# Performance work log

Measured on AMD Instinct MI355X. Metric: run time of the kernel, lower is better.

Reference implementation:

```python
import jax, jax.numpy as jnp
import numpy as np

NA, NO = 3, 85  # anchors per level, nc+5
OUT = NA * NO   # 255


def _p(key, shape):
    return jax.random.normal(key, shape, dtype=jnp.float32) * 0.02


def setup_inputs() -> dict:
    key = jax.random.key(0)
    ks = jax.random.split(key, 12)
    return {
        'x0': jax.random.normal(ks[0], (8, 128, 160, 160), jnp.float32),
        'x1': jax.random.normal(ks[1], (8, 256, 80, 80), jnp.float32),
        'x2': jax.random.normal(ks[2], (8, 512, 40, 40), jnp.float32),
        'x3': jax.random.normal(ks[3], (8, 1024, 20, 20), jnp.float32),
        # CLLABlock 1x1 convs (weight stored as [out_ch, in_ch])
        'w_conv1': _p(ks[4], (128, 128)), 'b_conv1': jnp.zeros((128,), jnp.float32),
        'w_conv2': _p(ks[5], (128, 256)), 'b_conv2': jnp.zeros((128,), jnp.float32),
        # CLLA q/k/v Linear layers (torch Linear: [out_feat, in_feat])
        'wq': _p(ks[6], (128, 128)), 'bq': jnp.zeros((128,), jnp.float32),
        'wk': _p(ks[7], (128, 128)), 'bk': jnp.zeros((128,), jnp.float32),
        'wv': _p(ks[8], (128, 128)), 'bv': jnp.zeros((128,), jnp.float32),
        # det head conv and extra level convs m[0], m[1]
        'w_det': _p(ks[9], (OUT, 128)), 'b_det': jnp.zeros((OUT,), jnp.float32),
        'wm0': _p(ks[10], (OUT, 512)), 'bm0': jnp.zeros((OUT,), jnp.float32),
        'wm1': _p(ks[11], (OUT, 1024)), 'bm1': jnp.zeros((OUT,), jnp.float32),
    }


def _conv1x1(x, w, b):
    # x: [b,c,h,w], w: [o,c]
    return jnp.einsum('bchw,oc->bohw', x, w) + b[None, :, None, None]


def _clla(f1, f2, wq, bq, wk, bk, wv, bv):
    # f1: [b,c,2H,2W] (fine), f2: [b,c,H,W] (coarse); range=2 -> pad=0
    b, c, H, W = f2.shape
    # torch loop: local[n] = f1[..., i::2, j::2], n = i*2+j, stacked on a new axis,
    # then permute(0,3,4,2,1) -> [b,H,W,4,c]
    loc = f1.reshape(b, c, H, 2, W, 2).transpose(0, 2, 4, 3, 5, 1).reshape(b, H, W, 4, c)
    x2_ = f2.transpose(0, 2, 3, 1)              # [b,H,W,c]
    q = x2_ @ wq.T + bq                          # [b,H,W,c]
    k = loc @ wk.T + bk                          # [b,H,W,4,c]
    v = loc @ wv.T + bv                          # [b,H,W,4,c]
    dots = jnp.einsum('bhwc,bhwnc->bhwn', q, k) / 2.0  # /range
    irr = 2.0 * jnp.mean(dots, axis=-1, keepdims=True) - dots
    att = jax.nn.softmax(irr, axis=-1)           # [b,H,W,4]
    out = jnp.einsum('bhwn,bhwnc->bhwc', att, v).transpose(0, 3, 1, 2)  # [b,c,H,W]
    return (out + f2) / 2.0


def _reshape_head(p):
    bs, _, ny, nx = p.shape
    return p.reshape(bs, NA, NO, ny, nx).transpose(0, 1, 3, 4, 2)  # [bs,na,ny,nx,no]


def reference(x0, x1, x2, x3,
              w_conv1, b_conv1, w_conv2, b_conv2,
              wq, bq, wk, bk, wv, bv,
              w_det, b_det, wm0, bm0, wm1, bm1):
    # training-mode forward of CLLADetect: returns raw head outputs p
    f1 = _conv1x1(x0, w_conv1, b_conv1)
    f2 = _conv1x1(x1, w_conv2, b_conv2)
    f = _clla(f1, f2, wq, bq, wk, bk, wv, bv)
    p0 = _reshape_head(_conv1x1(f, w_det, b_det))   # [8,3,80,80,85]
    p1 = _reshape_head(_conv1x1(x2, wm0, bm0))      # [8,3,40,40,85]
    p2 = _reshape_head(_conv1x1(x3, wm1, bm1))      # [8,3,20,20,85]
    return (p0, p1, p2)
```

## Files before the change

kernel.cpp:

```cpp
#include <hip/hip_runtime.h>

typedef unsigned short u16;
typedef unsigned int   u32;
typedef __bf16 bf16x8 __attribute__((ext_vector_type(8)));
typedef float  f32x4  __attribute__((ext_vector_type(4)));

__device__ __forceinline__ u16 f2bf(float f){
  u32 u = __float_as_uint(f);
  return (u16)((u + 0x7FFFu + ((u >> 16) & 1u)) >> 16);
}
__device__ __forceinline__ float bf2f(u16 h){ return __uint_as_float(((u32)h) << 16); }

#define WS_A1    0u
#define WS_WM0   196608u
#define WS_WM1   458752u
#define WS_WDVC  983040u
#define WS_C1    1048576u
#define WS_BM0   1051136u
#define WS_BM1   1052160u
#define WS_T     1053184u
#define WS_U     1184256u
#define WS_P     1184768u
#define WS_W6    1316352u
#define WS_U6    1381888u
#define WS_R     1382400u

__device__ __forceinline__ size_t wimg_off(int n, int k, int BN, int nK){
  int nt = n / BN, r = n % BN, kt = k >> 6;
  int slot = (((k & 63) >> 3) ^ (r & 7));
  return (size_t)(nt * nK + kt) * (size_t)(BN * 128) + (size_t)r * 128 + (slot << 4) + (k & 7) * 2;
}

__global__ __launch_bounds__(256) void prepA_k(const float* __restrict__ wq, const float* __restrict__ bq,
                                               const float* __restrict__ wc2, const float* __restrict__ bc2,
                                               const float* __restrict__ wk,  const float* __restrict__ wv,
                                               const float* __restrict__ wc1, const float* __restrict__ bc1,
                                               const float* __restrict__ bv,  char* ws)
{
  const int blk = blockIdx.x, j = threadIdx.x;
  if (blk < 128){
    int a = blk;
    float s = 0.f;
    for (int c = 0; c < 128; c++) s += wq[a * 128 + c] * wc2[c * 256 + j];
    ((float*)(ws + WS_T))[a * 256 + j] = s;
    if (j == 0){
      float su = bq[a];
      for (int c = 0; c < 128; c++) su += wq[a * 128 + c] * bc2[c];
      ((float*)(ws + WS_U))[a] = su;
    }
  } else if (blk < 256){
    int n = blk - 128;
    if (j < 128){
      float s = 0.f;
      for (int c = 0; c < 128; c++) s += wk[n * 128 + c] * wc1[c * 128 + j];
      ((float*)(ws + WS_P))[n * 128 + j] = s;
    }
  } else {
    int n = blk - 256;
    if (j < 128){
      float s = 0.f;
      for (int c = 0; c < 128; c++) s += wv[n * 128 + c] * wc1[c * 128 + j];
      ((float*)(ws + WS_W6))[n * 128 + j] = s;
    }
    if (j == 0){
      float s = bv[n];
      for (int c = 0; c < 128; c++) s += wv[n * 128 + c] * bc1[c];
      ((float*)(ws + WS_U6))[n] = s;
    }
  }
}

__global__ __launch_bounds__(256) void prep2_k(
    const float* __restrict__ wc2,
    const float* __restrict__ wdet, const float* __restrict__ bdet,
    const float* __restrict__ wm0, const float* __restrict__ bm0,
    const float* __restrict__ wm1, const float* __restrict__ bm1,
    const float* __restrict__ bc2, char* ws)
{
  const float* T  = (const float*)(ws + WS_T);
  const float* u  = (const float*)(ws + WS_U);
  const float* P  = (const float*)(ws + WS_P);
  const float* W6 = (const float*)(ws + WS_W6);
  const float* U6 = (const float*)(ws + WS_U6);
  int idx = blockIdx.x * 256 + threadIdx.x;
  if (idx < 98304){
    int n = idx >> 8, k = idx & 255;
    float s = 0.f;
    if (n < 128){
      for (int i = 0; i < 128; i++) s += P[i * 128 + n] * T[i * 256 + k];
      s *= 0.5f;
    } else if (n < 383){
      int oc = n - 128;
      for (int c = 0; c < 128; c++) s += wdet[oc * 128 + c] * wc2[c * 256 + k];
      s *= 0.5f;
    }
    *(u16*)(ws + WS_A1 + wimg_off(n, k, 128, 4)) = f2bf(s);
  } else if (idx < 98688){
    int n = idx - 98304;
    float s = 0.f;
    if (n < 128){
      for (int i = 0; i < 128; i++) s += P[i * 128 + n] * u[i];
      s *= 0.5f;
    } else if (n < 383){
      int oc = n - 128;
      float ss = 0.f;
      for (int c = 0; c < 128; c++) ss += wdet[oc * 128 + c] * (bc2[c] + U6[c]);
      s = bdet[oc] + 0.5f * ss;
    }
    ((float*)(ws + WS_C1))[n] = s;
  } else if (idx < 131456){
    int id = idx - 98688; int n = id >> 7, k = id & 127;
    float s = 0.f;
    if (n < 255){
      for (int c = 0; c < 128; c++) s += wdet[n * 128 + c] * W6[c * 128 + k];
      s *= 0.5f;
    }
    ((u16*)(ws + WS_WDVC))[n * 128 + k] = f2bf(s);
  } else if (idx < 262528){
    int id = idx - 131456; int n = id >> 9, k = id & 511;
    float s = (n < 255) ? wm0[n * 512 + k] : 0.f;
    *(u16*)(ws + WS_WM0 + wimg_off(n, k, 256, 8)) = f2bf(s);
  } else if (idx < 524672){
    int id = idx - 262528; int n = id >> 10, k = id & 1023;
    float s = (n < 255) ? wm1[n * 1024 + k] : 0.f;
    *(u16*)(ws + WS_WM1 + wimg_off(n, k, 256, 16)) = f2bf(s);
  } else if (idx < 525184){
    int id = idx - 524672;
    if (id < 256) ((float*)(ws + WS_BM0))[id] = (id < 255) ? bm0[id] : 0.f;
    else { int n = id - 256; ((float*)(ws + WS_BM1))[n] = (n < 255) ? bm1[n] : 0.f; }
  }
}

template<int Kd, int BM, int BN, int WM, int WN, int PPB, int Cin, int EPI, int ROWB>
__device__ __forceinline__ void gemm_body(char* lds, int mt, int nt,
                                          const float* __restrict__ Ap, const char* __restrict__ wimg,
                                          const float* __restrict__ bias, void* __restrict__ outp, long out_off)
{
  constexpr int nK = Kd / 64;
  constexpr int NV = BM / 16;
  char* ldsA = lds;
  char* ldsW = lds + BM * 128;
  const int t = threadIdx.x;
  const int lane = t & 63;
  const int wid = t >> 6;
  const int wm = wid / WN, wn = wid % WN;
  const int m0 = mt * BM, n0 = nt * BN;
  const int lr = lane & 15, lg = lane >> 4;
  f32x4 acc[4][4] = {};

  const int q = t & 3, chl = t >> 2;
  const int chunkA = chl >> 3, elo = (chl & 7) * 2;

  for (int kt = 0; kt < nK; kt++){
    {
      const int c = kt * 64 + chl;
      float4 v4[NV];
      #pragma unroll
      for (int v = 0; v < NV; v++){
        int pg = m0 + v * 16 + q * 4;
        int bb = pg / PPB, pp = pg - bb * PPB;
        v4[v] = *(const float4*)(Ap + (size_t)bb * Cin * PPB + (size_t)c * PPB + pp);
      }
      #pragma unroll
      for (int v = 0; v < NV; v++){
        #pragma unroll
        for (int e = 0; e < 4; e++){
          int pi = v * 16 + q * 4 + e;
          float val = ((const float*)&v4[v])[e];
          *(u16*)(ldsA + pi * 128 + ((chunkA ^ (pi & 7)) << 4) + elo) = f2bf(val);
        }
      }
    }
    {
      const char* srct = wimg + (size_t)(nt * nK + kt) * (BN * 128);
      #pragma unroll
      for (int it = 0; it < BN / 32; it++){
        int off = t * 16 + it * 4096;
        *(uint4*)(ldsW + off) = *(const uint4*)(srct + off);
      }
    }
    __syncthreads();
    #pragma unroll
    for (int ks = 0; ks < 2; ks++){
      bf16x8 af[4], bfr[4];
      #pragma unroll
      for (int i = 0; i < 4; i++){
        int r = wm * 64 + i * 16 + lr;
        af[i] = *(const bf16x8*)(ldsA + r * 128 + ((((ks << 2) + lg) ^ (r & 7)) << 4));
      }
      #pragma unroll
      for (int j = 0; j < 4; j++){
        int r = wn * 64 + j * 16 + lr;
        bfr[j] = *(const bf16x8*)(ldsW + r * 128 + ((((ks << 2) + lg) ^ (r & 7)) << 4));
      }
      #pragma unroll
      for (int i = 0; i < 4; i++)
        #pragma unroll
        for (int j = 0; j < 4; j++)
          acc[i][j] = __builtin_amdgcn_mfma_f32_16x16x32_bf16(af[i], bfr[j], acc[i][j], 0, 0, 0);
    }
    __syncthreads();
  }

  if constexpr (EPI == 0){
    u16* lds2 = (u16*)lds;
    #pragma unroll
    for (int j = 0; j < 4; j++){
      int nl = wn * 64 + j * 16 + lr;
      float bs = bias[n0 + nl];
      #pragma unroll
      for (int i = 0; i < 4; i++){
        #pragma unroll
        for (int r = 0; r < 4; r++){
          int ml = wm * 64 + i * 16 + lg * 4 + r;
          lds2[ml * 136 + nl] = f2bf(acc[i][j][r] + bs);
        }
      }
    }
    __syncthreads();
    char* outb = (char*)outp;
    #pragma unroll
    for (int it = 0; it < BM / 16; it++){
      int idx = it * 256 + t;
      int row = idx >> 4, c16 = idx & 15;
      *(uint4*)(outb + (size_t)(m0 + row) * ROWB + n0 * 2 + c16 * 16) =
          *(const uint4*)((const char*)lds2 + row * 272 + c16 * 16);
    }
  } else {
    #pragma unroll
    for (int j = 0; j < 4; j++){
      int nn = n0 + wn * 64 + j * 16 + lr;
      float bs = bias[nn];
      #pragma unroll
      for (int i = 0; i < 4; i++){
        #pragma unroll
        for (int r = 0; r < 4; r++){
          int mm = m0 + wm * 64 + i * 16 + lg * 4 + r;
          float v = acc[i][j][r] + bs;
          if (nn < 255){
            int b = mm / PPB, p = mm - b * PPB;
            int a = nn / 85, o = nn - a * 85;
            ((float*)outp)[out_off + ((size_t)(b * 3 + a) * PPB + p) * 85 + o] = v;
          }
        }
      }
    }
  }
}

__global__ __launch_bounds__(256) void gemms_k(const float* __restrict__ x1,
                                               const float* __restrict__ x2,
                                               const float* __restrict__ x3,
                                               char* __restrict__ ws,
                                               float* __restrict__ out)
{
  __shared__ char lds[40960];
  const int bid = blockIdx.x;
  if (bid < 50){
    gemm_body<1024, 64, 256, 1, 4, 400, 1024, 2, 0>(lds, bid, 0,
        x3, ws + WS_WM1, (const float*)(ws + WS_BM1), out, 16320000L);
  } else if (bid < 250){
    gemm_body<512, 64, 256, 1, 4, 1600, 512, 2, 0>(lds, bid - 50, 0,
        x2, ws + WS_WM0, (const float*)(ws + WS_BM0), out, 13056000L);
  } else {
    int b2 = bid - 250;
    gemm_body<256, 128, 128, 2, 2, 6400, 256, 0, 768>(lds, b2 / 3, b2 % 3,
        x1, ws + WS_A1, (const float*)(ws + WS_C1), ws + WS_R, 0L);
  }
}

__global__ __launch_bounds__(256) void clla_k(const float* __restrict__ x0,
                                              const char* __restrict__ ws,
                                              float* __restrict__ out)
{
  __shared__ char smem[29184];
  char* x0s = smem;
  char* rs  = smem + 16384;
  char* h0s = smem + 20480;
  float* stg = (float*)smem;

  const char* Rb   = ws + WS_R;
  const char* wdvi = ws + WS_WDVC;

  const int t = threadIdx.x;
  const int lane = t & 63, wid = t >> 6;
  const int lr = lane & 15, lg = lane >> 4;
  const int blk = blockIdx.x;
  const int b = blk / 400, rem = blk % 400;
  const int h = rem / 5, w0 = (rem % 5) * 16;
  const int c0 = b * 6400 + h * 80 + w0;
  const int pr = h * 80 + w0;

  {
    const int ch = t >> 1, r = t & 1;
    const float* gp = x0 + ((size_t)b * 128 + ch) * 25600
                    + (size_t)(2 * h + r) * 160 + 2 * w0;
    float4 v4[8];
    #pragma unroll
    for (int i = 0; i < 8; i++) v4[i] = *(const float4*)(gp + i * 4);
    const int chunk = ch >> 3, elo = (ch & 7) * 2;
    #pragma unroll
    for (int i = 0; i < 8; i++){
      #pragma unroll
      for (int e = 0; e < 4; e++){
        int j = i * 4 + e;
        int fr = ((j >> 1) << 2) + r * 2 + (j & 1);
        float val = ((const float*)&v4[i])[e];
        *(u16*)(x0s + fr * 256 + (((chunk ^ ((fr & 7) << 1)) & 15) << 4) + elo) = f2bf(val);
      }
    }
    const int lc2 = t >> 4, c2 = t & 15;
    *(uint4*)(rs + lc2 * 256 + (((c2 ^ ((lc2 & 7) << 1)) & 15) << 4)) =
        *(const uint4*)(Rb + (size_t)(c0 + lc2) * 768 + c2 * 16);
    #pragma unroll
    for (int i = 0; i < 2; i++){
      int idx = i * 256 + t;
      int row = idx >> 5, c16 = idx & 31;
      *(uint4*)(h0s + row * 544 + c16 * 16) =
          *(const uint4*)(Rb + (size_t)(c0 + row) * 768 + 256 + c16 * 16);
    }
  }
  __syncthreads();

  float myatt;
  {
    const int px = t >> 4, n = (t >> 2) & 3, cq2 = t & 3;
    const int fr = px * 4 + n;
    float d = 0.f;
    #pragma unroll
    for (int g = 0; g < 4; g++){
      int c = cq2 * 4 + g;
      bf16x8 rv = *(const bf16x8*)(rs  + px * 256 + (((c ^ ((px & 7) << 1)) & 15) << 4));
      bf16x8 fv = *(const bf16x8*)(x0s + fr * 256 + (((c ^ ((fr & 7) << 1)) & 15) << 4));
      #pragma unroll
      for (int e = 0; e < 8; e++) d += (float)rv[e] * (float)fv[e];
    }
    d += __shfl_xor(d, 1); d += __shfl_xor(d, 2);
    float s4 = d + __shfl_xor(d, 4); s4 += __shfl_xor(s4, 8);
    float irr = 0.5f * s4 - d;
    float mx = fmaxf(irr, __shfl_xor(irr, 4)); mx = fmaxf(mx, __shfl_xor(mx, 8));
    float e1 = __expf(irr - mx);
    float den = e1 + __shfl_xor(e1, 4); den += __shfl_xor(den, 8);
    myatt = e1 / den;
  }

  {
    const int px = t >> 4, cp = t & 15;
    float o[8];
    #pragma unroll
    for (int e = 0; e < 8; e++) o[e] = 0.f;
    #pragma unroll
    for (int n = 0; n < 4; n++){
      float a = __shfl(myatt, (t & 48) | (n << 2));
      int fr = px * 4 + n;
      bf16x8 fv = *(const bf16x8*)(x0s + fr * 256 + (((cp ^ ((fr & 7) << 1)) & 15) << 4));
      #pragma unroll
      for (int e = 0; e < 8; e++) o[e] += a * (float)fv[e];
    }
    uint4 wv_;
    wv_.x = (u32)f2bf(o[0]) | ((u32)f2bf(o[1]) << 16);
    wv_.y = (u32)f2bf(o[2]) | ((u32)f2bf(o[3]) << 16);
    wv_.z = (u32)f2bf(o[4]) | ((u32)f2bf(o[5]) << 16);
    wv_.w = (u32)f2bf(o[6]) | ((u32)f2bf(o[7]) << 16);
    *(uint4*)(rs + px * 256 + (((cp ^ ((px & 7) << 1)) & 15) << 4)) = wv_;
  }
  __syncthreads();

  {
    bf16x8 af[4];
    #pragma unroll
    for (int kt = 0; kt < 4; kt++){
      int chunk = kt * 4 + lg;
      af[kt] = *(const bf16x8*)(rs + lr * 256 + (((chunk ^ ((lr & 7) << 1)) & 15) << 4));
    }
    #pragma unroll
    for (int jj = 0; jj < 4; jj++){
      int jn = wid * 4 + jj;
      f32x4 acc = (f32x4){0.f, 0.f, 0.f, 0.f};
      #pragma unroll
      for (int kt = 0; kt < 4; kt++){
        bf16x8 bfr = *(const bf16x8*)(wdvi + (jn * 16 + lr) * 256 + (kt * 4 + lg) * 16);
        acc = __builtin_amdgcn_mfma_f32_16x16x32_bf16(af[kt], bfr, acc, 0, 0, 0);
      }
      int oc = jn * 16 + lr;
      if (oc < 255){
        int a = oc / 85, o = oc - a * 85;
        #pragma unroll
        for (int ri = 0; ri < 4; ri++){
          int px = lg * 4 + ri;
          float v = acc[ri] + bf2f(*(const u16*)(h0s + px * 544 + oc * 2));
          stg[a * 1360 + px * 85 + o] = v;
        }
      }
    }
  }
  __syncthreads();

  {
    #pragma unroll
    for (int it = 0; it < 4; it++){
      int idx = it * 256 + t;
      if (idx < 1020){
        int a = idx / 340, r4 = idx - a * 340;
        *(float4*)(out + ((size_t)(b * 3 + a) * 6400 + pr) * 85 + r4 * 4) =
            *(const float4*)(stg + a * 1360 + r4 * 4);
      }
    }
  }
}

extern "C" void kernel_launch(void* const* d_in, const int* in_sizes, int n_in,
                              void* d_out, int out_size, void* d_ws, size_t ws_size,
                              hipStream_t stream)
{
  (void)in_sizes; (void)n_in; (void)out_size; (void)ws_size;
  const float* x0  = (const float*)d_in[0];
  const float* x1  = (const float*)d_in[1];
  const float* x2  = (const float*)d_in[2];
  const float* x3  = (const float*)d_in[3];
  const float* wc1 = (const float*)d_in[4];  const float* bc1 = (const float*)d_in[5];
  const float* wc2 = (const float*)d_in[6];  const float* bc2 = (const float*)d_in[7];
  const float* wq  = (const float*)d_in[8];  const float* bq  = (const float*)d_in[9];
  const float* wk  = (const float*)d_in[10];
  const float* wv  = (const float*)d_in[12]; const float* bv  = (const float*)d_in[13];
  const float* wdt = (const float*)d_in[14]; const float* bdt = (const float*)d_in[15];
  const float* wm0 = (const float*)d_in[16]; const float* bm0 = (const float*)d_in[17];
  const float* wm1 = (const float*)d_in[18]; const float* bm1 = (const float*)d_in[19];
  char* ws = (char*)d_ws;
  float* out = (float*)d_out;

  prepA_k<<<384, 256, 0, stream>>>(wq, bq, wc2, bc2, wk, wv, wc1, bc1, bv, ws);
  prep2_k<<<2052, 256, 0, stream>>>(wc2, wdt, bdt, wm0, bm0, wm1, bm1, bc2, ws);
  gemms_k<<<1450, 256, 0, stream>>>(x1, x2, x3, ws, out);
  clla_k<<<3200, 256, 0, stream>>>(x0, ws, out);
}
```

Before: 123.9 us.

## Process four tiles per block in clla_k with register prefetch of next tile

clla_k now loops over four tiles per block instead of one, cutting the grid from 3200 to 800 blocks. The global loads for the next tile (x0 slice, R rows) go into registers right after the first barrier, so they overlap the attention and MFMA work of the current tile. The cost is higher register pressure from the prefetch buffers, an extra barrier per iteration, and fewer blocks in flight, which could reduce latency hiding across the GPU.

After: 129.8 us. 1.05x slower.

```diff
diff --git a/kernel.cpp b/kernel.cpp
--- a/kernel.cpp
+++ b/kernel.cpp
@@ -285,127 +285,149 @@
   const int t = threadIdx.x;
   const int lane = t & 63, wid = t >> 6;
   const int lr = lane & 15, lg = lane >> 4;
-  const int blk = blockIdx.x;
-  const int b = blk / 400, rem = blk % 400;
-  const int h = rem / 5, w0 = (rem % 5) * 16;
-  const int c0 = b * 6400 + h * 80 + w0;
-  const int pr = h * 80 + w0;
-
-  {
-    const int ch = t >> 1, r = t & 1;
+
+  const int ch = t >> 1, r = t & 1;
+  const int lc2 = t >> 4, c2 = t & 15;
+
+  float4 v4[8];
+  uint4  rsv, h0v[2];
+
+  auto load_tile = [&](int tl){
+    int b = tl / 400, rem = tl % 400;
+    int h = rem / 5, w0 = (rem % 5) * 16;
+    int c0 = b * 6400 + h * 80 + w0;
     const float* gp = x0 + ((size_t)b * 128 + ch) * 25600
                     + (size_t)(2 * h + r) * 160 + 2 * w0;
-    float4 v4[8];
     #pragma unroll
     for (int i = 0; i < 8; i++) v4[i] = *(const float4*)(gp + i * 4);
-    const int chunk = ch >> 3, elo = (ch & 7) * 2;
-    #pragma unroll
-    for (int i = 0; i < 8; i++){
-      #pragma unroll
-      for (int e = 0; e < 4; e++){
-        int j = i * 4 + e;
-        int fr = ((j >> 1) << 2) + r * 2 + (j & 1);
-        float val = ((const float*)&v4[i])[e];
-        *(u16*)(x0s + fr * 256 + (((chunk ^ ((fr & 7) << 1)) & 15) << 4) + elo) = f2bf(val);
-      }
-    }
-    const int lc2 = t >> 4, c2 = t & 15;
-    *(uint4*)(rs + lc2 * 256 + (((c2 ^ ((lc2 & 7) << 1)) & 15) << 4)) =
-        *(const uint4*)(Rb + (size_t)(c0 + lc2) * 768 + c2 * 16);
+    rsv = *(const uint4*)(Rb + (size_t)(c0 + lc2) * 768 + c2 * 16);
     #pragma unroll
     for (int i = 0; i < 2; i++){
       int idx = i * 256 + t;
       int row = idx >> 5, c16 = idx & 31;
-      *(uint4*)(h0s + row * 544 + c16 * 16) =
-          *(const uint4*)(Rb + (size_t)(c0 + row) * 768 + 256 + c16 * 16);
-    }
-  }
-  __syncthreads();
-
-  float myatt;
-  {
-    const int px = t >> 4, n = (t >> 2) & 3, cq2 = t & 3;
-    const int fr = px * 4 + n;
-    float d = 0.f;
-    #pragma unroll
-    for (int g = 0; g < 4; g++){
-      int c = cq2 * 4 + g;
-      bf16x8 rv = *(const bf16x8*)(rs  + px * 256 + (((c ^ ((px & 7) << 1)) & 15) << 4));
-      bf16x8 fv = *(const bf16x8*)(x0s + fr * 256 + (((c ^ ((fr & 7) << 1)) & 15) << 4));
-      #pragma unroll
-      for (int e = 0; e < 8; e++) d += (float)rv[e] * (float)fv[e];
-    }
-    d += __shfl_xor(d, 1); d += __shfl_xor(d, 2);
-    float s4 = d + __shfl_xor(d, 4); s4 += __shfl_xor(s4, 8);
-    float irr = 0.5f * s4 - d;
-    float mx = fmaxf(irr, __shfl_xor(irr, 4)); mx = fmaxf(mx, __shfl_xor(mx, 8));
-    float e1 = __expf(irr - mx);
-    float den = e1 + __shfl_xor(e1, 4); den += __shfl_xor(den, 8);
-    myatt = e1 / den;
-  }
-
-  {
-    const int px = t >> 4, cp = t & 15;
-    float o[8];
-    #pragma unroll
-    for (int e = 0; e < 8; e++) o[e] = 0.f;
-    #pragma unroll
-    for (int n = 0; n < 4; n++){
-      float a = __shfl(myatt, (t & 48) | (n << 2));
-      int fr = px * 4 + n;
-      bf16x8 fv = *(const bf16x8*)(x0s + fr * 256 + (((cp ^ ((fr & 7) << 1)) & 15) << 4));
-      #pragma unroll
-      for (int e = 0; e < 8; e++) o[e] += a * (float)fv[e];
-    }
-    uint4 wv_;
-    wv_.x = (u32)f2bf(o[0]) | ((u32)f2bf(o[1]) << 16);
-    wv_.y = (u32)f2bf(o[2]) | ((u32)f2bf(o[3]) << 16);
-    wv_.z = (u32)f2bf(o[4]) | ((u32)f2bf(o[5]) << 16);
-    wv_.w = (u32)f2bf(o[6]) | ((u32)f2bf(o[7]) << 16);
-    *(uint4*)(rs + px * 256 + (((cp ^ ((px & 7) << 1)) & 15) << 4)) = wv_;
-  }
-  __syncthreads();
-
-  {
-    bf16x8 af[4];
-    #pragma unroll
-    for (int kt = 0; kt < 4; kt++){
-      int chunk = kt * 4 + lg;
-      af[kt] = *(const bf16x8*)(rs + lr * 256 + (((chunk ^ ((lr & 7) << 1)) & 15) << 4));
-    }
-    #pragma unroll
-    for (int jj = 0; jj < 4; jj++){
-      int jn = wid * 4 + jj;
-      f32x4 acc = (f32x4){0.f, 0.f, 0.f, 0.f};
+      h0v[i] = *(const uint4*)(Rb + (size_t)(c0 + row) * 768 + 256 + c16 * 16);
+    }
+  };
+
+  const int tile0 = blockIdx.x * 4;
+  load_tile(tile0);
+
+  for (int it = 0; it < 4; it++){
+    const int tl = tile0 + it;
+    const int b = tl / 400, rem = tl % 400;
+    const int h = rem / 5, w0 = (rem % 5) * 16;
+    const int pr = h * 80 + w0;
+
+    {
+      const int chunk = ch >> 3, elo = (ch & 7) * 2;
+      #pragma unroll
+      for (int i = 0; i < 8; i++){
+        #pragma unroll
+        for (int e = 0; e < 4; e++){
+          int j = i * 4 + e;
+          int fr = ((j >> 1) << 2) + r * 2 + (j & 1);
+          float val = ((const float*)&v4[i])[e];
+          *(u16*)(x0s + fr * 256 + (((chunk ^ ((fr & 7) << 1)) & 15) << 4) + elo) = f2bf(val);
+        }
+      }
+      *(uint4*)(rs + lc2 * 256 + (((c2 ^ ((lc2 & 7) << 1)) & 15) << 4)) = rsv;
+      #pragma unroll
+      for (int i = 0; i < 2; i++){
+        int idx = i * 256 + t;
+        int row = idx >> 5, c16 = idx & 31;
+        *(uint4*)(h0s + row * 544 + c16 * 16) = h0v[i];
+      }
+    }
+    __syncthreads();
+
+    if (it < 3) load_tile(tl + 1);
+
+    float myatt;
+    {
+      const int px = t >> 4, n = (t >> 2) & 3, cq2 = t & 3;
+      const int fr = px * 4 + n;
+      float d = 0.f;
+      #pragma unroll
+      for (int g = 0; g < 4; g++){
+        int c = cq2 * 4 + g;
+        bf16x8 rv = *(const bf16x8*)(rs  + px * 256 + (((c ^ ((px & 7) << 1)) & 15) << 4));
+        bf16x8 fv = *(const bf16x8*)(x0s + fr * 256 + (((c ^ ((fr & 7) << 1)) & 15) << 4));
+        #pragma unroll
+        for (int e = 0; e < 8; e++) d += (float)rv[e] * (float)fv[e];
+      }
+      d += __shfl_xor(d, 1); d += __shfl_xor(d, 2);
+      float s4 = d + __shfl_xor(d, 4); s4 += __shfl_xor(s4, 8);
+      float irr = 0.5f * s4 - d;
+      float mx = fmaxf(irr, __shfl_xor(irr, 4)); mx = fmaxf(mx, __shfl_xor(mx, 8));
+      float e1 = __expf(irr - mx);
+      float den = e1 + __shfl_xor(e1, 4); den += __shfl_xor(den, 8);
+      myatt = e1 / den;
+    }
+
+    {
+      const int px = t >> 4, cp = t & 15;
+      float o[8];
+      #pragma unroll
+      for (int e = 0; e < 8; e++) o[e] = 0.f;
+      #pragma unroll
+      for (int n = 0; n < 4; n++){
+        float a = __shfl(myatt, (t & 48) | (n << 2));
+        int fr = px * 4 + n;
+        bf16x8 fv = *(const bf16x8*)(x0s + fr * 256 + (((cp ^ ((fr & 7) << 1)) & 15) << 4));
+        #pragma unroll
+        for (int e = 0; e < 8; e++) o[e] += a * (float)fv[e];
+      }
+      uint4 wv_;
+      wv_.x = (u32)f2bf(o[0]) | ((u32)f2bf(o[1]) << 16);
+      wv_.y = (u32)f2bf(o[2]) | ((u32)f2bf(o[3]) << 16);
+      wv_.z = (u32)f2bf(o[4]) | ((u32)f2bf(o[5]) << 16);
+      wv_.w = (u32)f2bf(o[6]) | ((u32)f2bf(o[7]) << 16);
+      *(uint4*)(rs + px * 256 + (((cp ^ ((px & 7) << 1)) & 15) << 4)) = wv_;
+    }
+    __syncthreads();
+
+    {
+      bf16x8 af[4];
       #pragma unroll
       for (int kt = 0; kt < 4; kt++){
-        bf16x8 bfr = *(const bf16x8*)(wdvi + (jn * 16 + lr) * 256 + (kt * 4 + lg) * 16);
-        acc = __builtin_amdgcn_mfma_f32_16x16x32_bf16(af[kt], bfr, acc, 0, 0, 0);
-      }
-      int oc = jn * 16 + lr;
-      if (oc < 255){
-        int a = oc / 85, o = oc - a * 85;
-        #pragma unroll
-        for (int ri = 0; ri < 4; ri++){
-          int px = lg * 4 + ri;
-          float v = acc[ri] + bf2f(*(const u16*)(h0s + px * 544 + oc * 2));
-          stg[a * 1360 + px * 85 + o] = v;
-        }
-      }
-    }
-  }
-  __syncthreads();
-
-  {
-    #pragma unroll
-    for (int it = 0; it < 4; it++){
-      int idx = it * 256 + t;
-      if (idx < 1020){
-        int a = idx / 340, r4 = idx - a * 340;
-        *(float4*)(out + ((size_t)(b * 3 + a) * 6400 + pr) * 85 + r4 * 4) =
-            *(const float4*)(stg + a * 1360 + r4 * 4);
-      }
-    }
+        int chunk = kt * 4 + lg;
+        af[kt] = *(const bf16x8*)(rs + lr * 256 + (((chunk ^ ((lr & 7) << 1)) & 15) << 4));
+      }
+      #pragma unroll
+      for (int jj = 0; jj < 4; jj++){
+        int jn = wid * 4 + jj;
+        f32x4 acc = (f32x4){0.f, 0.f, 0.f, 0.f};
+        #pragma unroll
+        for (int kt = 0; kt < 4; kt++){
+          bf16x8 bfr = *(const bf16x8*)(wdvi + (jn * 16 + lr) * 256 + (kt * 4 + lg) * 16);
+          acc = __builtin_amdgcn_mfma_f32_16x16x32_bf16(af[kt], bfr, acc, 0, 0, 0);
+        }
+        int oc = jn * 16 + lr;
+        if (oc < 255){
+          int a = oc / 85, o = oc - a * 85;
+          #pragma unroll
+          for (int ri = 0; ri < 4; ri++){
+            int px = lg * 4 + ri;
+            float v = acc[ri] + bf2f(*(const u16*)(h0s + px * 544 + oc * 2));
+            stg[a * 1360 + px * 85 + o] = v;
+          }
+        }
+      }
+    }
+    __syncthreads();
+
+    {
+      #pragma unroll
+      for (int i2 = 0; i2 < 4; i2++){
+        int idx = i2 * 256 + t;
+        if (idx < 1020){
+          int a = idx / 340, r4 = idx - a * 340;
+          *(float4*)(out + ((size_t)(b * 3 + a) * 6400 + pr) * 85 + r4 * 4) =
+              *(const float4*)(stg + a * 1360 + r4 * 4);
+        }
+      }
+    }
+    __syncthreads();
   }
 }
 
@@ -432,5 +454,5 @@
   prepA_k<<<384, 256, 0, stream>>>(wq, bq, wc2, bc2, wk, wv, wc1, bc1, bv, ws);
   prep2_k<<<2052, 256, 0, stream>>>(wc2, wdt, bdt, wm0, bm0, wm1, bm1, bc2, ws);
   gemms_k<<<1450, 256, 0, stream>>>(x1, x2, x3, ws, out);
-  clla_k<<<3200, 256, 0, stream>>>(x0, ws, out);
-}
+  clla_k<<<800, 256, 0, stream>>>(x0, ws, out);
+}
```

## Pre-transpose x0 to bf16 tile image in separate kernel for CLLA

Applied to the files above, without the earlier changes.

Adds a kernel that reads x0 with wide coalesced loads, converts it to bf16 and writes it to workspace in the exact swizzled per-block tile layout that clla_k uses. clla_k then copies its tile with contiguous 16-byte loads instead of doing strided fp32 reads and scalar LDS scatters. This is meant to improve global access efficiency and cut conversion work inside the CLLA kernel. In exchange it adds an extra kernel launch and a round trip through global memory for a bf16 copy of x0 (about 52MB written and read back).

New measurement: 161.1 us. +30.0%, slower.

```diff
diff --git a/kernel.cpp b/kernel.cpp
--- a/kernel.cpp
+++ b/kernel.cpp
@@ -24,11 +24,16 @@
 #define WS_W6    1316352u
 #define WS_U6    1381888u
 #define WS_R     1382400u
+#define WS_X0T   40704000u
 
 __device__ __forceinline__ size_t wimg_off(int n, int k, int BN, int nK){
   int nt = n / BN, r = n % BN, kt = k >> 6;
   int slot = (((k & 63) >> 3) ^ (r & 7));
   return (size_t)(nt * nK + kt) * (size_t)(BN * 128) + (size_t)r * 128 + (slot << 4) + (k & 7) * 2;
+}
+
+__device__ __forceinline__ int x0t_addr(int fr, int c ){
+  return ((c >> 3) << 13) + fr * 128 + ((((c & 7) ^ (fr & 7)) & 7) << 4);
 }
 
 __global__ __launch_bounds__(256) void prepA_k(const float* __restrict__ wq, const float* __restrict__ bq,
@@ -131,6 +136,50 @@
   }
 }
 
+__global__ __launch_bounds__(256) void xpose_k(const float* __restrict__ x0, char* __restrict__ ws)
+{
+  __shared__ char lds[40960];
+  const int t = threadIdx.x;
+  const int bid = blockIdx.x;
+  const int b = bid / 80, h = bid % 80;
+  const int c2 = t >> 3;
+  const int r  = (t >> 2) & 1;
+  const int wh = (t >> 1) & 1;
+  const int hp = t & 1;
+  const int p0 = wh * 80 + hp * 40;
+
+  for (int h2 = 0; h2 < 2; h2++){
+    const int ch0 = h2 * 64 + c2 * 2;
+    const float* g0 = x0 + ((size_t)b * 128 + ch0) * 25600 + (size_t)(2 * h + r) * 160 + p0;
+    const float* g1 = g0 + 25600;
+    float4 va[10], vb[10];
+    #pragma unroll
+    for (int i = 0; i < 10; i++){ va[i] = *(const float4*)(g0 + i * 4); vb[i] = *(const float4*)(g1 + i * 4); }
+    if (h2 == 1) __syncthreads();
+    const int chunk7 = (c2 * 2) >> 3;
+    const int elo = ((c2 * 2) & 7) * 2;
+    #pragma unroll
+    for (int i = 0; i < 10; i++){
+      #pragma unroll
+      for (int e = 0; e < 4; e++){
+        int p = p0 + i * 4 + e;
+        int tw = p >> 5, jj = p & 31;
+        int fr = ((jj >> 1) << 2) + r * 2 + (jj & 1);
+        u32 pk = (u32)f2bf(((const float*)&va[i])[e]) | ((u32)f2bf(((const float*)&vb[i])[e]) << 16);
+        *(u32*)(lds + tw * 8192 + fr * 128 + ((((chunk7) ^ (fr & 7)) & 7) << 4) + elo) = pk;
+      }
+    }
+    __syncthreads();
+    char* dstb = ws + WS_X0T + (size_t)(b * 400 + h * 5) * 16384 + h2 * 8192;
+    #pragma unroll
+    for (int k = 0; k < 10; k++){
+      int idx = k * 256 + t;
+      int tw = idx >> 9, off = idx & 511;
+      *(uint4*)(dstb + (size_t)tw * 16384 + off * 16) = *(const uint4*)(lds + tw * 8192 + off * 16);
+    }
+  }
+}
+
 template<int Kd, int BM, int BN, int WM, int WN, int PPB, int Cin, int EPI, int ROWB>
 __device__ __forceinline__ void gemm_body(char* lds, int mt, int nt,
                                           const float* __restrict__ Ap, const char* __restrict__ wimg,
@@ -269,8 +318,7 @@
   }
 }
 
-__global__ __launch_bounds__(256) void clla_k(const float* __restrict__ x0,
-                                              const char* __restrict__ ws,
+__global__ __launch_bounds__(256) void clla_k(const char* __restrict__ ws,
                                               float* __restrict__ out)
 {
   __shared__ char smem[29184];
@@ -292,22 +340,11 @@
   const int pr = h * 80 + w0;
 
   {
-    const int ch = t >> 1, r = t & 1;
-    const float* gp = x0 + ((size_t)b * 128 + ch) * 25600
-                    + (size_t)(2 * h + r) * 160 + 2 * w0;
-    float4 v4[8];
-    #pragma unroll
-    for (int i = 0; i < 8; i++) v4[i] = *(const float4*)(gp + i * 4);
-    const int chunk = ch >> 3, elo = (ch & 7) * 2;
-    #pragma unroll
-    for (int i = 0; i < 8; i++){
-      #pragma unroll
-      for (int e = 0; e < 4; e++){
-        int j = i * 4 + e;
-        int fr = ((j >> 1) << 2) + r * 2 + (j & 1);
-        float val = ((const float*)&v4[i])[e];
-        *(u16*)(x0s + fr * 256 + (((chunk ^ ((fr & 7) << 1)) & 15) << 4) + elo) = f2bf(val);
-      }
+    const char* src = ws + WS_X0T + (size_t)blk * 16384;
+    #pragma unroll
+    for (int k = 0; k < 4; k++){
+      int off = k * 4096 + t * 16;
+      *(uint4*)(x0s + off) = *(const uint4*)(src + off);
     }
     const int lc2 = t >> 4, c2 = t & 15;
     *(uint4*)(rs + lc2 * 256 + (((c2 ^ ((lc2 & 7) << 1)) & 15) << 4)) =
@@ -331,7 +368,7 @@
     for (int g = 0; g < 4; g++){
       int c = cq2 * 4 + g;
       bf16x8 rv = *(const bf16x8*)(rs  + px * 256 + (((c ^ ((px & 7) << 1)) & 15) << 4));
-      bf16x8 fv = *(const bf16x8*)(x0s + fr * 256 + (((c ^ ((fr & 7) << 1)) & 15) << 4));
+      bf16x8 fv = *(const bf16x8*)(x0s + x0t_addr(fr, c));
       #pragma unroll
       for (int e = 0; e < 8; e++) d += (float)rv[e] * (float)fv[e];
     }
@@ -353,7 +390,7 @@
     for (int n = 0; n < 4; n++){
       float a = __shfl(myatt, (t & 48) | (n << 2));
       int fr = px * 4 + n;
-      bf16x8 fv = *(const bf16x8*)(x0s + fr * 256 + (((cp ^ ((fr & 7) << 1)) & 15) << 4));
+      bf16x8 fv = *(const bf16x8*)(x0s + x0t_addr(fr, cp));
       #pragma unroll
       for (int e = 0; e < 8; e++) o[e] += a * (float)fv[e];
     }
@@ -431,6 +468,7 @@
 
   prepA_k<<<384, 256, 0, stream>>>(wq, bq, wc2, bc2, wk, wv, wc1, bc1, bv, ws);
   prep2_k<<<2052, 256, 0, stream>>>(wc2, wdt, bdt, wm0, bm0, wm1, bm1, bc2, ws);
+  xpose_k<<<640, 256, 0, stream>>>(x0, ws);
   gemms_k<<<1450, 256, 0, stream>>>(x1, x2, x3, ws, out);
-  clla_k<<<3200, 256, 0, stream>>>(x0, ws, out);
-}
+  clla_k<<<3200, 256, 0, stream>>>(ws, out);
+}
```
